# Optimization experiments

Measured on AMD Instinct MI355X. Metric: run time of the kernel, lower is better.

The kernel has to match this reference:

```python
import jax, jax.numpy as jnp
import numpy as np

B, S, N = 8, 2048, 1024

def setup_inputs() -> dict:
    key = jax.random.key(0)
    k1, k2, k3 = jax.random.split(key, 3)
    outer = jax.random.normal(k1, (B, S, N), dtype=jnp.float32)
    extended_attention_mask = jnp.zeros((B, 1, S), dtype=jnp.float32)
    # torch Linear init scale ~ 1/sqrt(n)
    sc = 1.0 / np.sqrt(N)
    Wk = jax.random.normal(k2, (N, N), dtype=jnp.float32) * sc
    bk = jnp.zeros((N,), dtype=jnp.float32)
    Wq = jax.random.normal(k3, (N, N), dtype=jnp.float32) * sc
    bq = jnp.zeros((N,), dtype=jnp.float32)
    return {"outer": outer, "extended_attention_mask": extended_attention_mask,
            "Wk": Wk, "bk": bk, "Wq": Wq, "bq": bq}

def reference(outer, extended_attention_mask, Wk, bk, Wq, bq):
    # k = sigmoid(outer @ Wk^T + bk), q = sigmoid(outer @ Wq^T + bq)
    k = jax.nn.sigmoid(jnp.einsum('bsn,mn->bsm', outer, Wk) + bk)  # [B,S,N]
    q = jax.nn.sigmoid(jnp.einsum('bsn,mn->bsm', outer, Wq) + bq)  # [B,S,N]
    # scores: q @ k^T + mask -> [B,S,S]
    s = jnp.einsum('bqn,bkn->bqk', q, k) + extended_attention_mask
    attn = jax.nn.softmax(s, axis=-1)
    out = jnp.einsum('bqk,bkn->bqn', attn, outer)  # [B,S,N]
    return out.sum(-1)  # [B,S]
```

## Files before the change

kernel.cpp:

```cpp
#include <hip/hip_runtime.h>
#include <hip/hip_bf16.h>

#define BB 8
#define SS 2048
#define NN 1024
#define MT (BB*SS)
#define NPC 32
#define NT 16

typedef __attribute__((ext_vector_type(8))) short bf16x8;
typedef __attribute__((ext_vector_type(4))) float f32x4;
typedef unsigned short u16;
typedef unsigned int u32;

__device__ __forceinline__ u16 f2bf(float f) {
  u32 u = __float_as_uint(f);
  u += 0x7fff + ((u >> 16) & 1);
  return (u16)(u >> 16);
}
__device__ __forceinline__ float bf2f(u16 h) {
  return __uint_as_float(((u32)h) << 16);
}

typedef __attribute__((address_space(1))) void GV;
typedef __attribute__((address_space(3))) void LV;
__device__ __forceinline__ void cp16(const void* g, void* l) {
  __builtin_amdgcn_global_load_lds((GV*)g, (LV*)l, 16, 0, 0);
}

#define WAIT8 asm volatile("s_waitcnt vmcnt(8)" ::: "memory")
#define WAIT0 asm volatile("s_waitcnt vmcnt(0)" ::: "memory")
#define LGKM0 asm volatile("s_waitcnt lgkmcnt(0)" ::: "memory")
#define BARX  __builtin_amdgcn_s_barrier()
#define SCB0  __builtin_amdgcn_sched_barrier(0)

__global__ __launch_bounds__(256) void prep_x_kernel(const float* __restrict__ outer,
                                                     const float* __restrict__ mask,
                                                     u16* __restrict__ Xb,
                                                     float* __restrict__ r,
                                                     float* __restrict__ kb) {
  int w = threadIdx.x >> 6, lane = threadIdx.x & 63;
  int row = blockIdx.x * 4 + w;
  const float4* src = (const float4*)(outer + (size_t)row * NN);
  ushort4* dst = (ushort4*)(Xb + (size_t)row * NN);
  float s = 0.f;
#pragma unroll
  for (int u = 0; u < 4; u++) {
    int idx = lane + u * 64;
    float4 v = src[idx];
    ushort4 o;
    o.x = f2bf(v.x); o.y = f2bf(v.y); o.z = f2bf(v.z); o.w = f2bf(v.w);
    dst[idx] = o;
    s += (v.x + v.y) + (v.z + v.w);
  }
#pragma unroll
  for (int off = 1; off < 64; off <<= 1) s += __shfl_xor(s, off);
  if (lane == 0) { r[row] = s; kb[row] = mask[row]; }
}

__global__ __launch_bounds__(256) void prep_w_kernel(const float* __restrict__ Wq,
                                                     const float* __restrict__ Wk,
                                                     const float* __restrict__ bq,
                                                     const float* __restrict__ bk,
                                                     u16* __restrict__ Wb,
                                                     float* __restrict__ bb) {
  int idx = blockIdx.x * 256 + threadIdx.x;
  int e = idx * 4;
  int rowm = e >> 10;
  int col = e & 1023;
  const float* srcp = (rowm < NN) ? (Wq + (size_t)rowm * NN + col)
                                  : (Wk + (size_t)(rowm - NN) * NN + col);
  float4 v = *(const float4*)srcp;
  ushort4 o; o.x = f2bf(v.x); o.y = f2bf(v.y); o.z = f2bf(v.z); o.w = f2bf(v.w);
  *(ushort4*)(Wb + (size_t)e) = o;
  if (idx < 2 * NN) bb[idx] = (idx < NN) ? bq[idx] : bk[idx - NN];
}

template<int LDG>
__device__ __forceinline__ void gemm_core(const u16* gA, const u16* gB,
                                          u16* lds, int tid,
                                          f32x4 (&acc)[8][4]) {
  const int lane = tid & 63, w = tid >> 6;
  const int wr = w >> 2, wc = w & 3;
  const int l15 = lane & 15, quad = lane >> 4, xq = l15 & 7;
  const int lr = lane >> 3, lc = lane & 7;
  const int sslot = lc ^ lr;
  const int so0 = (quad ^ xq) * 8;
  const int so1 = ((4 + quad) ^ xq) * 8;

  const u16* gAr = gA + (size_t)(wr * 128 + wc * 8 + lr) * LDG + sslot * 8;
  const u16* gBr = gB + (size_t)(wc * 64 + wr * 8 + lr) * LDG + sslot * 8;

  u16* dA = lds + wr * 8192 + (wc * 64 + lane) * 8;
  u16* dB = lds + 16384 + wc * 4096 + wr * 512 + lane * 8;
  const u16* pA = lds + wr * 8192 + l15 * 64;
  const u16* pB = lds + 16384 + wc * 4096 + l15 * 64;

  bf16x8 af[4][2], bf0[2][2], bf1[2][2];

  auto STA = [&](int buf, int lo, int kt) {
    cp16(gAr + (size_t)lo * 32 * LDG + kt * 64, dA + buf * 32768 + lo * 2048);
  };
  auto STB = [&](int buf, int lb, int kt) {
    cp16(gBr + (size_t)lb * 16 * LDG + kt * 64, dB + buf * 32768 + lb * 1024);
  };
  auto RAF = [&](int buf, int ih) {
#pragma unroll
    for (int i2 = 0; i2 < 4; ++i2) {
      const u16* p = pA + buf * 32768 + (ih * 64 + i2 * 16) * 64;
      af[i2][0] = *(const bf16x8*)(p + so0);
      af[i2][1] = *(const bf16x8*)(p + so1);
    }
  };
  auto RBF = [&](bf16x8 (&bf)[2][2], int buf, int jh) {
#pragma unroll
    for (int j2 = 0; j2 < 2; ++j2) {
      const u16* p = pB + buf * 32768 + (jh * 2 + j2) * 1024;
      bf[j2][0] = *(const bf16x8*)(p + so0);
      bf[j2][1] = *(const bf16x8*)(p + so1);
    }
  };
  auto MQ = [&](int ih, int jh, bf16x8 (&bf)[2][2]) {
    __builtin_amdgcn_s_setprio(1);
#pragma unroll
    for (int ks = 0; ks < 2; ++ks)
#pragma unroll
      for (int i2 = 0; i2 < 4; ++i2)
#pragma unroll
        for (int j2 = 0; j2 < 2; ++j2)
          acc[ih * 4 + i2][jh * 2 + j2] =
              __builtin_amdgcn_mfma_f32_16x16x32_bf16(af[i2][ks], bf[j2][ks],
                                                      acc[ih * 4 + i2][jh * 2 + j2], 0, 0, 0);
    __builtin_amdgcn_s_setprio(0);
  };

  STA(0, 0, 0); STA(0, 1, 0); STB(0, 0, 0); STB(0, 1, 0);
  STB(0, 2, 0); STB(0, 3, 0); STA(0, 2, 0); STA(0, 3, 0);
  STA(1, 0, 1); STA(1, 1, 1); STB(1, 2, 1); STB(1, 3, 1);
  STB(1, 0, 1); STB(1, 1, 1);

  auto TILE = [&](int t, int buf) {
    const int nb = buf ^ 1;
    if (t < NT - 1) { STA(nb, 2, t + 1); STA(nb, 3, t + 1); WAIT8; }
    else            { WAIT0; }
    BARX;
    RAF(buf, 0); RBF(bf0, buf, 0);
    LGKM0; SCB0;
    MQ(0, 0, bf0);
    SCB0;
    RBF(bf1, buf, 1);
    BARX; LGKM0; SCB0;
    MQ(0, 1, bf1);
    SCB0;
    RAF(buf, 1);
    if (t < NT - 2) { STA(buf, 0, t + 2); STA(buf, 1, t + 2); }
    BARX; LGKM0; SCB0;
    MQ(1, 1, bf1);
    if (t < NT - 2) { STB(buf, 2, t + 2); STB(buf, 3, t + 2);
                      STB(buf, 0, t + 2); STB(buf, 1, t + 2); }
    BARX; SCB0;
    MQ(1, 0, bf0);
  };

#pragma unroll 1
  for (int tt = 0; tt < 8; ++tt) {
    TILE(2 * tt,     0);
    TILE(2 * tt + 1, 1);
  }
}

__global__ __launch_bounds__(512, 2) void gemm1_kernel(const u16* __restrict__ X,
                                                       const u16* __restrict__ W,
                                                       const float* __restrict__ bb,
                                                       u16* __restrict__ C,
                                                       float* __restrict__ kb) {
  __shared__ u16 lds[2 * 32768];
  int bid = blockIdx.x;
  int xcd = bid & 7, idx = bid >> 3;
  int tm = xcd * 8 + (idx & 7);
  int tn = idx >> 3;
  int tid = threadIdx.x;
  f32x4 acc[8][4] = {};
  gemm_core<1024>(X + (size_t)tm * 256 * 1024, W + (size_t)tn * 256 * 1024,
                  lds, tid, acc);

  int lane = tid & 63, w = tid >> 6;
  int wr = w >> 2, wc = w & 3, l15 = lane & 15, quad = lane >> 4;
  int colb = tn * 256 + wc * 64 + l15;
  bool khalf = (tn >= 4);
  int rowb = tm * 256 + wr * 128 + quad * 4;
#pragma unroll
  for (int i = 0; i < 8; ++i) {
    float rsum[4] = {0.f, 0.f, 0.f, 0.f};
#pragma unroll
    for (int j = 0; j < 4; ++j) {
      int col = colb + j * 16;
      float bias = bb[col];
#pragma unroll
      for (int rg = 0; rg < 4; ++rg) {
        int row = rowb + i * 16 + rg;
        float v = acc[i][j][rg] + bias;
        float sg = 1.0f / (1.0f + __expf(-v));
        u16 h = f2bf(sg - 0.5f);
        C[(size_t)row * 2048 + col] = h;
        rsum[rg] += bf2f(h);
      }
    }
    if (khalf) {
#pragma unroll
      for (int rg = 0; rg < 4; ++rg) {
        float s = rsum[rg];
#pragma unroll
        for (int off = 1; off < 16; off <<= 1) s += __shfl_xor(s, off);
        if (l15 == 0) atomicAdd(&kb[rowb + i * 16 + rg], 0.5f * s);
      }
    }
  }
}

__global__ __launch_bounds__(512, 2) void flash_kernel(const u16* __restrict__ Cq,
                                                       const float* __restrict__ kb,
                                                       const float* __restrict__ r,
                                                       float* __restrict__ pm,
                                                       float* __restrict__ pl,
                                                       float* __restrict__ pt) {
  __shared__ u16 lds[2 * 32768];
  int bid = blockIdx.x;
  int b = bid & 7;
  int idx = bid >> 3;
  int qt = idx >> 3;
  int kc = idx & 7;
  int tid = threadIdx.x;
  f32x4 acc[8][4] = {};
  gemm_core<2048>(Cq + (size_t)(b * SS + qt * 256) * 2048,
                  Cq + (size_t)(b * SS + kc * 256) * 2048 + 1024,
                  lds, tid, acc);

  int lane = tid & 63, w = tid >> 6;
  int wr = w >> 2, wc = w & 3, l15 = lane & 15, quad = lane >> 4;
  float kbv[4], rv[4];
  int colg = b * SS + kc * 256 + wc * 64 + l15;
#pragma unroll
  for (int j = 0; j < 4; ++j) { kbv[j] = kb[colg + j * 16]; rv[j] = r[colg + j * 16]; }
  int chunk = kc * 4 + wc;
  int rowb = b * SS + qt * 256 + wr * 128 + quad * 4;
#pragma unroll
  for (int i = 0; i < 8; ++i) {
#pragma unroll
    for (int rg = 0; rg < 4; ++rg) {
      float lg[4];
      float tmax = -1e30f;
#pragma unroll
      for (int j = 0; j < 4; ++j) { lg[j] = acc[i][j][rg] + kbv[j]; tmax = fmaxf(tmax, lg[j]); }
#pragma unroll
      for (int off = 1; off < 16; off <<= 1) tmax = fmaxf(tmax, __shfl_xor(tmax, off));
      float rs = 0.f, rt = 0.f;
#pragma unroll
      for (int j = 0; j < 4; ++j) {
        float p = __expf(lg[j] - tmax);
        rs += p; rt += p * rv[j];
      }
#pragma unroll
      for (int off = 1; off < 16; off <<= 1) { rs += __shfl_xor(rs, off); rt += __shfl_xor(rt, off); }
      if (l15 == 0) {
        int grow = rowb + i * 16 + rg;
        pm[(size_t)grow * NPC + chunk] = tmax;
        pl[(size_t)grow * NPC + chunk] = rs;
        pt[(size_t)grow * NPC + chunk] = rt;
      }
    }
  }
}

__global__ __launch_bounds__(256) void fixup_kernel(const float* __restrict__ pm,
                                                    const float* __restrict__ pl,
                                                    const float* __restrict__ pt,
                                                    float* __restrict__ out) {
  int row = blockIdx.x * 256 + threadIdx.x;
  float Mx = -1e30f;
#pragma unroll
  for (int c = 0; c < NPC; c++) Mx = fmaxf(Mx, pm[row * NPC + c]);
  float L = 0.f, T = 0.f;
#pragma unroll
  for (int c = 0; c < NPC; c++) {
    float a = __expf(pm[row * NPC + c] - Mx);
    L += pl[row * NPC + c] * a;
    T += pt[row * NPC + c] * a;
  }
  out[row] = T / L;
}

extern "C" void kernel_launch(void* const* d_in, const int* in_sizes, int n_in,
                              void* d_out, int out_size, void* d_ws, size_t ws_size,
                              hipStream_t stream) {
  const float* outer = (const float*)d_in[0];
  const float* mask  = (const float*)d_in[1];
  const float* Wk    = (const float*)d_in[2];
  const float* bk    = (const float*)d_in[3];
  const float* Wq    = (const float*)d_in[4];
  const float* bq    = (const float*)d_in[5];
  float* out = (float*)d_out;

  char* ws = (char*)d_ws;
  size_t off = 0;
  auto alloc = [&](size_t bytes) -> void* {
    void* p = ws + off;
    off = (off + bytes + 255) & ~(size_t)255;
    return p;
  };
  u16* Xb  = (u16*)alloc((size_t)MT * NN * 2);
  u16* Wb  = (u16*)alloc((size_t)2048 * NN * 2);
  u16* Cq  = (u16*)alloc((size_t)MT * 2048 * 2);
  float* bb = (float*)alloc(2048 * 4);
  float* rr = (float*)alloc((size_t)MT * 4);
  float* kb = (float*)alloc((size_t)MT * 4);
  float* pm = (float*)alloc((size_t)MT * NPC * 4);
  float* pl = (float*)alloc((size_t)MT * NPC * 4);
  float* pt = (float*)alloc((size_t)MT * NPC * 4);

  prep_x_kernel<<<dim3(MT / 4), dim3(256), 0, stream>>>(outer, mask, Xb, rr, kb);
  prep_w_kernel<<<dim3(2048), dim3(256), 0, stream>>>(Wq, Wk, bq, bk, Wb, bb);
  gemm1_kernel<<<dim3(512), dim3(512), 0, stream>>>(Xb, Wb, bb, Cq, kb);
  flash_kernel<<<dim3(512), dim3(512), 0, stream>>>(Cq, kb, rr, pm, pl, pt);
  fixup_kernel<<<dim3(MT / 256), dim3(256), 0, stream>>>(pm, pl, pt, out);
}
```

Baseline: 266.6 us.

## Merge prep kernels and restructure GEMM tile schedule with fewer barriers

The two input-conversion kernels are merged into one launch that dispatches on block index, removing a kernel launch and its gap. The GEMM tile loop is rescheduled: both B fragment sets are read up front with a partial lgkmcnt wait, and the next-tile A and B global-to-LDS copies are issued together after a single barrier instead of being spread across several barriers. This cuts barrier count per tile and lets LDS reads overlap MFMA, but the buffer reuse ordering must still keep fragment reads ahead of overwrites.

```diff
diff --git a/kernel.cpp b/kernel.cpp
--- a/kernel.cpp
+++ b/kernel.cpp
@@ -30,50 +30,53 @@
 
 #define WAIT8 asm volatile("s_waitcnt vmcnt(8)" ::: "memory")
 #define WAIT0 asm volatile("s_waitcnt vmcnt(0)" ::: "memory")
+#define LGKM4 asm volatile("s_waitcnt lgkmcnt(4)" ::: "memory")
 #define LGKM0 asm volatile("s_waitcnt lgkmcnt(0)" ::: "memory")
 #define BARX  __builtin_amdgcn_s_barrier()
 #define SCB0  __builtin_amdgcn_sched_barrier(0)
 
-__global__ __launch_bounds__(256) void prep_x_kernel(const float* __restrict__ outer,
-                                                     const float* __restrict__ mask,
-                                                     u16* __restrict__ Xb,
-                                                     float* __restrict__ r,
-                                                     float* __restrict__ kb) {
-  int w = threadIdx.x >> 6, lane = threadIdx.x & 63;
-  int row = blockIdx.x * 4 + w;
-  const float4* src = (const float4*)(outer + (size_t)row * NN);
-  ushort4* dst = (ushort4*)(Xb + (size_t)row * NN);
-  float s = 0.f;
-#pragma unroll
-  for (int u = 0; u < 4; u++) {
-    int idx = lane + u * 64;
-    float4 v = src[idx];
-    ushort4 o;
-    o.x = f2bf(v.x); o.y = f2bf(v.y); o.z = f2bf(v.z); o.w = f2bf(v.w);
-    dst[idx] = o;
-    s += (v.x + v.y) + (v.z + v.w);
-  }
-#pragma unroll
-  for (int off = 1; off < 64; off <<= 1) s += __shfl_xor(s, off);
-  if (lane == 0) { r[row] = s; kb[row] = mask[row]; }
-}
-
-__global__ __launch_bounds__(256) void prep_w_kernel(const float* __restrict__ Wq,
-                                                     const float* __restrict__ Wk,
-                                                     const float* __restrict__ bq,
-                                                     const float* __restrict__ bk,
-                                                     u16* __restrict__ Wb,
-                                                     float* __restrict__ bb) {
-  int idx = blockIdx.x * 256 + threadIdx.x;
-  int e = idx * 4;
-  int rowm = e >> 10;
-  int col = e & 1023;
-  const float* srcp = (rowm < NN) ? (Wq + (size_t)rowm * NN + col)
-                                  : (Wk + (size_t)(rowm - NN) * NN + col);
-  float4 v = *(const float4*)srcp;
-  ushort4 o; o.x = f2bf(v.x); o.y = f2bf(v.y); o.z = f2bf(v.z); o.w = f2bf(v.w);
-  *(ushort4*)(Wb + (size_t)e) = o;
-  if (idx < 2 * NN) bb[idx] = (idx < NN) ? bq[idx] : bk[idx - NN];
+__global__ __launch_bounds__(256) void prep_kernel(const float* __restrict__ outer,
+                                                   const float* __restrict__ mask,
+                                                   const float* __restrict__ Wq,
+                                                   const float* __restrict__ Wk,
+                                                   const float* __restrict__ bq,
+                                                   const float* __restrict__ bk,
+                                                   u16* __restrict__ Xb,
+                                                   float* __restrict__ r,
+                                                   float* __restrict__ kb,
+                                                   u16* __restrict__ Wb,
+                                                   float* __restrict__ bb) {
+  int bid = blockIdx.x;
+  if (bid < 4096) {
+    int w = threadIdx.x >> 6, lane = threadIdx.x & 63;
+    int row = bid * 4 + w;
+    const float4* src = (const float4*)(outer + (size_t)row * NN);
+    ushort4* dst = (ushort4*)(Xb + (size_t)row * NN);
+    float s = 0.f;
+#pragma unroll
+    for (int u = 0; u < 4; u++) {
+      int idx = lane + u * 64;
+      float4 v = src[idx];
+      ushort4 o;
+      o.x = f2bf(v.x); o.y = f2bf(v.y); o.z = f2bf(v.z); o.w = f2bf(v.w);
+      dst[idx] = o;
+      s += (v.x + v.y) + (v.z + v.w);
+    }
+#pragma unroll
+    for (int off = 1; off < 64; off <<= 1) s += __shfl_xor(s, off);
+    if (lane == 0) { r[row] = s; kb[row] = mask[row]; }
+  } else {
+    int idx = (bid - 4096) * 256 + threadIdx.x;
+    int e = idx * 4;
+    int rowm = e >> 10;
+    int col = e & 1023;
+    const float* srcp = (rowm < NN) ? (Wq + (size_t)rowm * NN + col)
+                                    : (Wk + (size_t)(rowm - NN) * NN + col);
+    float4 v = *(const float4*)srcp;
+    ushort4 o; o.x = f2bf(v.x); o.y = f2bf(v.y); o.z = f2bf(v.z); o.w = f2bf(v.w);
+    *(ushort4*)(Wb + (size_t)e) = o;
+    if (idx < 2 * NN) bb[idx] = (idx < NN) ? bq[idx] : bk[idx - NN];
+  }
 }
 
 template<int LDG>
@@ -135,30 +138,28 @@
   };
 
   STA(0, 0, 0); STA(0, 1, 0); STB(0, 0, 0); STB(0, 1, 0);
-  STB(0, 2, 0); STB(0, 3, 0); STA(0, 2, 0); STA(0, 3, 0);
-  STA(1, 0, 1); STA(1, 1, 1); STB(1, 2, 1); STB(1, 3, 1);
-  STB(1, 0, 1); STB(1, 1, 1);
+  STA(0, 2, 0); STA(0, 3, 0); STB(0, 2, 0); STB(0, 3, 0);
+  STA(1, 0, 1); STA(1, 1, 1); STB(1, 0, 1); STB(1, 1, 1);
+  STB(1, 2, 1); STB(1, 3, 1);
 
   auto TILE = [&](int t, int buf) {
     const int nb = buf ^ 1;
     if (t < NT - 1) { STA(nb, 2, t + 1); STA(nb, 3, t + 1); WAIT8; }
     else            { WAIT0; }
     BARX;
-    RAF(buf, 0); RBF(bf0, buf, 0);
+    RAF(buf, 0); RBF(bf0, buf, 0); RBF(bf1, buf, 1);
+    LGKM4; SCB0;
+    MQ(0, 0, bf0);
     LGKM0; SCB0;
-    MQ(0, 0, bf0);
-    SCB0;
-    RBF(bf1, buf, 1);
-    BARX; LGKM0; SCB0;
     MQ(0, 1, bf1);
     SCB0;
     RAF(buf, 1);
-    if (t < NT - 2) { STA(buf, 0, t + 2); STA(buf, 1, t + 2); }
-    BARX; LGKM0; SCB0;
+    BARX;
+    if (t < NT - 2) { STA(buf, 0, t + 2); STA(buf, 1, t + 2);
+                      STB(buf, 0, t + 2); STB(buf, 1, t + 2);
+                      STB(buf, 2, t + 2); STB(buf, 3, t + 2); }
+    LGKM0; SCB0;
     MQ(1, 1, bf1);
-    if (t < NT - 2) { STB(buf, 2, t + 2); STB(buf, 3, t + 2);
-                      STB(buf, 0, t + 2); STB(buf, 1, t + 2); }
-    BARX; SCB0;
     MQ(1, 0, bf0);
   };
 
@@ -318,8 +319,8 @@
   float* pl = (float*)alloc((size_t)MT * NPC * 4);
   float* pt = (float*)alloc((size_t)MT * NPC * 4);
 
-  prep_x_kernel<<<dim3(MT / 4), dim3(256), 0, stream>>>(outer, mask, Xb, rr, kb);
-  prep_w_kernel<<<dim3(2048), dim3(256), 0, stream>>>(Wq, Wk, bq, bk, Wb, bb);
+  prep_kernel<<<dim3(6144), dim3(256), 0, stream>>>(outer, mask, Wq, Wk, bq, bk,
+                                                    Xb, rr, kb, Wb, bb);
   gemm1_kernel<<<dim3(512), dim3(512), 0, stream>>>(Xb, Wb, bb, Cq, kb);
   flash_kernel<<<dim3(512), dim3(512), 0, stream>>>(Cq, kb, rr, pm, pl, pt);
   fixup_kernel<<<dim3(MT / 256), dim3(256), 0, stream>>>(pm, pl, pt, out);
```

After: 261.2 us. -2.0%, faster.
